# Performance work log

Hardware: AMD Instinct MI355X
Metric: run time of the kernel (lower is better)

Reference implementation:

```python
import jax, jax.numpy as jnp
import numpy as np

B, L, D = 2, 2048, 1024
H, DK, DV = 16, 64, 64
EPS = 1e-6


def setup_inputs() -> dict:
    key = jax.random.key(0)
    ks = jax.random.split(key, 7)
    s = 0.02
    return {
        "x": jax.random.normal(ks[0], (B, L, D), dtype=jnp.float32),
        "Wq": jax.random.normal(ks[1], (D, H * DK), dtype=jnp.float32) * s,
        "Wk": jax.random.normal(ks[2], (D, H * DK), dtype=jnp.float32) * s,
        "Wv": jax.random.normal(ks[3], (D, H * DV), dtype=jnp.float32) * s,
        "Wo": jax.random.normal(ks[4], (H * DV, D), dtype=jnp.float32) * s,
        "ln_gamma": jnp.ones((D,), dtype=jnp.float32),
        "ln_beta": jnp.zeros((D,), dtype=jnp.float32),
    }


def reference(x, Wq, Wk, Wv, Wo, ln_gamma, ln_beta):
    temp = jnp.asarray(DK, x.dtype) ** 0.5
    # projections -> [B, H, L, Dh]
    q = (x @ Wq).reshape(B, L, H, DK).transpose(0, 2, 1, 3)
    k = (x @ Wk).reshape(B, L, H, DK).transpose(0, 2, 1, 3)
    v = (x @ Wv).reshape(B, L, H, DV).transpose(0, 2, 1, 3)
    # naive attention: explicit [B,H,L,L] scores (dropout rate 0 -> identity)
    scores = jnp.einsum("bhqd,bhkd->bhqk", q / temp, k)
    attn = jax.nn.softmax(scores, axis=-1)
    o = jnp.einsum("bhqk,bhkd->bhqd", attn, v)
    o = o.transpose(0, 2, 1, 3).reshape(B, L, H * DV)
    out = o @ Wo + x  # residual
    # LayerNorm(eps=1e-6)
    mu = jnp.mean(out, axis=-1, keepdims=True)
    var = jnp.var(out, axis=-1, keepdims=True)
    return (out - mu) * jax.lax.rsqrt(var + EPS) * ln_gamma + ln_beta
```

## Files before the change

### kernel.cpp

```cpp
#include <hip/hip_runtime.h>


typedef __bf16 bf16;
typedef __bf16 bf16x2 __attribute__((ext_vector_type(2)));
typedef __bf16 bf16x4 __attribute__((ext_vector_type(4)));
typedef __bf16 bf16x8 __attribute__((ext_vector_type(8)));
typedef float floatx4 __attribute__((ext_vector_type(4)));
typedef int intx4 __attribute__((ext_vector_type(4)));

#define MFMA16(a, b, c) __builtin_amdgcn_mfma_f32_16x16x32_bf16((a), (b), (c), 0, 0, 0)

__device__ __forceinline__ void gll16(const bf16* g, bf16* l) {
  __builtin_amdgcn_global_load_lds((const __attribute__((address_space(1))) void*)g,
                                   (__attribute__((address_space(3))) void*)l, 16, 0, 0);
}

__global__ __launch_bounds__(256) void k_prep_x(const float* __restrict__ x, bf16* __restrict__ xb) {
  const int i = (blockIdx.x * 256 + threadIdx.x) * 4;
  const float4 v = *reinterpret_cast<const float4*>(x + i);
  bf16x4 o = {(bf16)v.x, (bf16)v.y, (bf16)v.z, (bf16)v.w};
  *reinterpret_cast<bf16x4*>(xb + i) = o;
}

__global__ __launch_bounds__(256) void k_prep_w(const float* __restrict__ Wq, const float* __restrict__ Wk,
                                                const float* __restrict__ Wv, const float* __restrict__ Wo,
                                                bf16* __restrict__ WT) {
  __shared__ float tile[32][33];
  const int z = blockIdx.z;
  const float* W = (z == 0) ? Wq : (z == 1) ? Wk : (z == 2) ? Wv : Wo;
  const int n0 = blockIdx.x * 32, k0 = blockIdx.y * 32;
  const int tx = threadIdx.x, ty = threadIdx.y;
#pragma unroll
  for (int j = 0; j < 32; j += 8)
    tile[ty + j][tx] = W[(size_t)(k0 + ty + j) * 1024 + n0 + tx];
  __syncthreads();
#pragma unroll
  for (int j = 0; j < 32; j += 8)
    WT[(size_t)(z * 1024 + n0 + ty + j) * 1024 + k0 + tx] = (bf16)tile[tx][ty + j];
}

template <int MODE>
__global__ __launch_bounds__(256) void k_gemm(const bf16* __restrict__ A, const bf16* __restrict__ Bt,
                                              const float* __restrict__ X, float* __restrict__ Y,
                                              bf16* __restrict__ QB, bf16* __restrict__ KB,
                                              bf16* __restrict__ VTB) {
  __shared__ __align__(16) bf16 As[2 * 128 * 64];
  __shared__ __align__(16) bf16 Bs[2 * 128 * 64];
  const int t = threadIdx.x;
  const int lane = t & 63, wv = t >> 6;
  const int qd = lane >> 4, col = lane & 15;
  const int c7 = col & 7;
  const int wm = wv >> 1, wn = wv & 1;
  const int m0 = blockIdx.x * 128, n0 = blockIdx.y * 128;
  const int srow = wv * 8 + (lane >> 3);
  const int scol = ((lane & 7) ^ (lane >> 3)) * 8;
  const bf16* Ag = A + (size_t)(m0 + srow) * 1024 + scol;
  const bf16* Bg = Bt + (size_t)(n0 + srow) * 1024 + scol;

  floatx4 acc[4][4] = {};

#define GSTAGE(ktv, buf)                                                                            \
  do {                                                                                              \
    _Pragma("unroll") for (int rd = 0; rd < 4; rd++) {                                              \
      gll16(Ag + (size_t)rd * 32 * 1024 + (ktv), As + (buf) * 8192 + (rd * 32 + wv * 8) * 64);      \
      gll16(Bg + (size_t)rd * 32 * 1024 + (ktv), Bs + (buf) * 8192 + (rd * 32 + wv * 8) * 64);      \
    }                                                                                               \
  } while (0)

#define GCOMP(buf)                                                                                  \
  do {                                                                                              \
    const bf16* as_ = As + (buf) * 8192;                                                            \
    const bf16* bs_ = Bs + (buf) * 8192;                                                            \
    _Pragma("unroll") for (int ks = 0; ks < 2; ks++) {                                              \
      bf16x8 af[4], bfr[4];                                                                         \
      _Pragma("unroll") for (int i = 0; i < 4; i++)                                                 \
        af[i] = *reinterpret_cast<const bf16x8*>(as_ + (wm * 64 + i * 16 + col) * 64 +              \
                                                 ((ks * 4 + qd) ^ c7) * 8);                         \
      _Pragma("unroll") for (int i = 0; i < 4; i++)                                                 \
        bfr[i] = *reinterpret_cast<const bf16x8*>(bs_ + (wn * 64 + i * 16 + col) * 64 +             \
                                                  ((ks * 4 + qd) ^ c7) * 8);                        \
      _Pragma("unroll") for (int i = 0; i < 4; i++)                                                 \
        _Pragma("unroll") for (int j = 0; j < 4; j++)                                               \
          acc[i][j] = MFMA16(af[i], bfr[j], acc[i][j]);                                             \
    }                                                                                               \
  } while (0)

  GSTAGE(0, 0);
  asm volatile("s_waitcnt vmcnt(0)" ::: "memory");
  __syncthreads();

  for (int kt = 0; kt < 1024; kt += 128) {
    GSTAGE(kt + 64, 1);
    GCOMP(0);
    asm volatile("s_waitcnt vmcnt(0)" ::: "memory");
    __syncthreads();
    if (kt + 128 < 1024) GSTAGE(kt + 128, 0);
    GCOMP(1);
    asm volatile("s_waitcnt vmcnt(0)" ::: "memory");
    __syncthreads();
  }
#undef GSTAGE
#undef GCOMP

#pragma unroll
  for (int i = 0; i < 4; i++) {
#pragma unroll
    for (int j = 0; j < 4; j++) {
      const int mb = m0 + wm * 64 + i * 16 + qd * 4;
      const int n = n0 + wn * 64 + j * 16 + col;
      if (MODE == 0) {
        const int seg = n >> 10;
        const int h = (n & 1023) >> 6, dd = n & 63;
#pragma unroll
        for (int r = 0; r < 4; r++) {
          const int m = mb + r;
          const int bb = m >> 11, l = m & 2047;
          const float v = acc[i][j][r];
          if (seg == 0)
            QB[((size_t)(bb * 16 + h) * 2048 + l) * 64 + dd] = (bf16)(v * 0.18033688f);
          else if (seg == 1)
            KB[((size_t)(bb * 16 + h) * 2048 + l) * 64 + dd] = (bf16)v;
          else
            VTB[((size_t)(bb * 16 + h) * 64 + dd) * 2048 + l] = (bf16)v;
        }
      } else {
#pragma unroll
        for (int r = 0; r < 4; r++) {
          const int m = mb + r;
          Y[(size_t)m * 1024 + n] = acc[i][j][r] + X[(size_t)m * 1024 + n];
        }
      }
    }
  }
}

__global__ __launch_bounds__(256) void k_attn(const bf16* __restrict__ QB, const bf16* __restrict__ KB,
                                              const bf16* __restrict__ VTB, bf16* __restrict__ PO0,
                                              bf16* __restrict__ PO1, float* __restrict__ LS) {
  __shared__ __align__(16) bf16 Ks[3][64 * 64];
  __shared__ __align__(16) bf16 Vs[3][64 * 64];
  const int t = threadIdx.x;
  const int lane = t & 63, wv = t >> 6;
  const int qd = lane >> 4, col = lane & 15;
  const int c7 = col & 7;
  const int bh = blockIdx.y;
  const int z = blockIdx.z;
  const int qr = blockIdx.x * 128 + wv * 32;
  const int lrow0 = wv * 8 + (lane >> 3);
  const int scol = ((lane & 7) ^ (lane >> 3)) * 8;
  const int kg0 = ((lrow0 >> 5) << 5) + (((lrow0 >> 2) & 3) << 3) + (((lrow0 >> 4) & 1) << 2) + (lrow0 & 3);
  const int r1 = lrow0 + 32;
  const int kg1 = ((r1 >> 5) << 5) + (((r1 >> 2) & 3) << 3) + (((r1 >> 4) & 1) << 2) + (r1 & 3);
  const bf16* Kg0 = KB + ((size_t)bh * 2048 + kg0) * 64 + scol;
  const bf16* Kg1 = KB + ((size_t)bh * 2048 + kg1) * 64 + scol;
  const bf16* Vg0 = VTB + ((size_t)bh * 64 + lrow0) * 2048 + scol;
  const bf16* Vg1 = VTB + ((size_t)bh * 64 + lrow0 + 32) * 2048 + scol;

  bf16x8 bQ[2][2];
#pragma unroll
  for (int qt = 0; qt < 2; qt++)
#pragma unroll
    for (int s = 0; s < 2; s++)
      bQ[qt][s] = *reinterpret_cast<const bf16x8*>(QB + ((size_t)bh * 2048 + qr + qt * 16 + col) * 64 + s * 32 + qd * 8);

  floatx4 oacc[2][4] = {};
  float lsum[2] = {0.f, 0.f};
  floatx4 scur[2][4];
  int pk[2][4][2];

#define STAGE(bu, ti)                                                  \
  do {                                                                 \
    gll16(Kg0 + (size_t)(ti) * 4096, &Ks[bu][(wv * 8) * 64]);          \
    gll16(Kg1 + (size_t)(ti) * 4096, &Ks[bu][(32 + wv * 8) * 64]);     \
    gll16(Vg0 + (ti) * 64, &Vs[bu][(wv * 8) * 64]);                    \
    gll16(Vg1 + (ti) * 64, &Vs[bu][(32 + wv * 8) * 64]);               \
  } while (0)

#define QK(bu)                                                                                      \
  do {                                                                                              \
    const bf16* ks_ = Ks[bu];                                                                       \
    _Pragma("unroll") for (int nt = 0; nt < 4; nt++) {                                              \
      bf16x8 a0 = *reinterpret_cast<const bf16x8*>(ks_ + (nt * 16 + col) * 64 + (qd ^ c7) * 8);     \
      bf16x8 a1 = *reinterpret_cast<const bf16x8*>(ks_ + (nt * 16 + col) * 64 + ((4 + qd) ^ c7) * 8); \
      _Pragma("unroll") for (int qt = 0; qt < 2; qt++) {                                            \
        floatx4 zz = {0.f, 0.f, 0.f, 0.f};                                                          \
        zz = MFMA16(a0, bQ[qt][0], zz);                                                             \
        zz = MFMA16(a1, bQ[qt][1], zz);                                                             \
        scur[qt][nt] = zz;                                                                          \
      }                                                                                             \
    }                                                                                               \
  } while (0)

#define EXPPACK()                                                                               \
  do {                                                                                          \
    _Pragma("unroll") for (int qt = 0; qt < 2; qt++) {                                          \
      _Pragma("unroll") for (int nt = 0; nt < 4; nt++) {                                        \
        const float e0 = __builtin_amdgcn_exp2f(scur[qt][nt][0]);                               \
        const float e1 = __builtin_amdgcn_exp2f(scur[qt][nt][1]);                               \
        const float e2 = __builtin_amdgcn_exp2f(scur[qt][nt][2]);                               \
        const float e3 = __builtin_amdgcn_exp2f(scur[qt][nt][3]);                               \
        lsum[qt] += (e0 + e1) + (e2 + e3);                                                      \
        bf16x2 p01, p23;                                                                        \
        p01[0] = (bf16)e0; p01[1] = (bf16)e1;                                                   \
        p23[0] = (bf16)e2; p23[1] = (bf16)e3;                                                   \
        pk[qt][nt][0] = __builtin_bit_cast(int, p01);                                           \
        pk[qt][nt][1] = __builtin_bit_cast(int, p23);                                           \
      }                                                                                         \
    }                                                                                           \
  } while (0)

#define PV(bu)                                                                                      \
  do {                                                                                              \
    const bf16* vs_ = Vs[bu];                                                                       \
    bf16x8 bV[4][2];                                                                                \
    _Pragma("unroll") for (int nd = 0; nd < 4; nd++) {                                              \
      bV[nd][0] = *reinterpret_cast<const bf16x8*>(vs_ + (nd * 16 + col) * 64 + (qd ^ c7) * 8);     \
      bV[nd][1] = *reinterpret_cast<const bf16x8*>(vs_ + (nd * 16 + col) * 64 + ((4 + qd) ^ c7) * 8); \
    }                                                                                               \
    _Pragma("unroll") for (int qt = 0; qt < 2; qt++) {                                              \
      _Pragma("unroll") for (int s = 0; s < 2; s++) {                                               \
        intx4 w;                                                                                    \
        w[0] = pk[qt][2 * s][0]; w[1] = pk[qt][2 * s][1];                                           \
        w[2] = pk[qt][2 * s + 1][0]; w[3] = pk[qt][2 * s + 1][1];                                   \
        const bf16x8 aP = __builtin_bit_cast(bf16x8, w);                                            \
        _Pragma("unroll") for (int nd = 0; nd < 4; nd++)                                            \
          oacc[qt][nd] = MFMA16(aP, bV[nd][s], oacc[qt][nd]);                                       \
      }                                                                                             \
    }                                                                                               \
  } while (0)

#define ITER(cur, prv, ti)                                             \
  do {                                                                 \
    asm volatile("s_waitcnt vmcnt(4)" ::: "memory");                   \
    __builtin_amdgcn_s_barrier();                                      \
    EXPPACK();                                                         \
    QK(cur);                                                           \
    PV(prv);                                                           \
    __builtin_amdgcn_s_barrier();                                      \
    STAGE(prv, ((ti) + 2 <= t0 + 15) ? ((ti) + 2) : (t0 + 15));        \
  } while (0)

  const int t0 = z * 16;
  STAGE(0, t0);
  STAGE(1, t0 + 1);
  asm volatile("s_waitcnt vmcnt(4)" ::: "memory");
  __builtin_amdgcn_s_barrier();
  QK(0);
  __builtin_amdgcn_s_barrier();
  STAGE(2, t0 + 2);
  for (int j = 1; j < 16; j += 3) {
    ITER(1, 0, t0 + j);
    ITER(2, 1, t0 + j + 1);
    ITER(0, 2, t0 + j + 2);
  }
  EXPPACK();
  PV(0);

#pragma unroll
  for (int qt = 0; qt < 2; qt++) {
    lsum[qt] += __shfl_xor(lsum[qt], 16);
    lsum[qt] += __shfl_xor(lsum[qt], 32);
  }
  if (qd == 0) {
#pragma unroll
    for (int qt = 0; qt < 2; qt++)
      LS[(size_t)z * 65536 + (size_t)bh * 2048 + qr + qt * 16 + col] = lsum[qt];
  }
  bf16* PO = z ? PO1 : PO0;
  const int bb = bh >> 4, h = bh & 15;
#pragma unroll
  for (int qt = 0; qt < 2; qt++) {
#pragma unroll
    for (int r = 0; r < 4; r++) {
      const size_t m = (size_t)bb * 2048 + qr + qt * 16 + qd * 4 + r;
#pragma unroll
      for (int nd = 0; nd < 4; nd++)
        PO[m * 1024 + h * 64 + nd * 16 + col] = (bf16)(oacc[qt][nd][r]);
    }
  }
#undef STAGE
#undef QK
#undef EXPPACK
#undef PV
#undef ITER
}

__global__ __launch_bounds__(256) void k_comb(const bf16* __restrict__ PO0, const bf16* __restrict__ PO1,
                                              const float* __restrict__ LS, bf16* __restrict__ OB) {
  const size_t idx = ((size_t)blockIdx.x * 256 + threadIdx.x) * 4;
  const int m = (int)(idx >> 10), c = (int)(idx & 1023);
  const int bb = m >> 11, l = m & 2047, h = c >> 6;
  const int bh = bb * 16 + h;
  const float linv = 1.f / (LS[(size_t)bh * 2048 + l] + LS[65536 + (size_t)bh * 2048 + l]);
  const bf16x4 a = *reinterpret_cast<const bf16x4*>(PO0 + idx);
  const bf16x4 b = *reinterpret_cast<const bf16x4*>(PO1 + idx);
  bf16x4 o;
#pragma unroll
  for (int i = 0; i < 4; i++) o[i] = (bf16)(((float)a[i] + (float)b[i]) * linv);
  *reinterpret_cast<bf16x4*>(OB + idx) = o;
}

__global__ __launch_bounds__(256) void k_ln(const float* __restrict__ Yin, const float* __restrict__ gamma,
                                            const float* __restrict__ beta, float* __restrict__ out) {
  __shared__ float red[8];
  const int row = blockIdx.x, t = threadIdx.x;
  const float4 v = *reinterpret_cast<const float4*>(Yin + (size_t)row * 1024 + t * 4);
  float s = v.x + v.y + v.z + v.w;
  float ss = v.x * v.x + v.y * v.y + v.z * v.z + v.w * v.w;
#pragma unroll
  for (int d = 1; d < 64; d <<= 1) {
    s += __shfl_xor(s, d);
    ss += __shfl_xor(ss, d);
  }
  if ((t & 63) == 0) {
    red[t >> 6] = s;
    red[4 + (t >> 6)] = ss;
  }
  __syncthreads();
  s = red[0] + red[1] + red[2] + red[3];
  ss = red[4] + red[5] + red[6] + red[7];
  const float mu = s * (1.f / 1024.f);
  const float var = ss * (1.f / 1024.f) - mu * mu;
  const float rs = rsqrtf(var + 1e-6f);
  const float4 g = *reinterpret_cast<const float4*>(gamma + t * 4);
  const float4 bt = *reinterpret_cast<const float4*>(beta + t * 4);
  float4 o;
  o.x = (v.x - mu) * rs * g.x + bt.x;
  o.y = (v.y - mu) * rs * g.y + bt.y;
  o.z = (v.z - mu) * rs * g.z + bt.z;
  o.w = (v.w - mu) * rs * g.w + bt.w;
  *reinterpret_cast<float4*>(out + (size_t)row * 1024 + t * 4) = o;
}

extern "C" void kernel_launch(void* const* d_in, const int* in_sizes, int n_in,
                              void* d_out, int out_size, void* d_ws, size_t ws_size,
                              hipStream_t stream) {
  (void)in_sizes; (void)n_in; (void)out_size; (void)ws_size;
  const float* x = (const float*)d_in[0];
  const float* Wq = (const float*)d_in[1];
  const float* Wk = (const float*)d_in[2];
  const float* Wv = (const float*)d_in[3];
  const float* Wo = (const float*)d_in[4];
  const float* gamma = (const float*)d_in[5];
  const float* beta = (const float*)d_in[6];

  char* ws = (char*)d_ws;
  const size_t MB = 1ull << 20;
  bf16* XB = (bf16*)(ws);
  bf16* PO0 = (bf16*)(ws);
  bf16* OB = (bf16*)(ws);
  bf16* WT = (bf16*)(ws + 8 * MB);
  bf16* QB = (bf16*)(ws + 16 * MB);
  bf16* KB = (bf16*)(ws + 24 * MB);
  bf16* VTB = (bf16*)(ws + 32 * MB);
  bf16* PO1 = (bf16*)(ws + 40 * MB);
  float* LS = (float*)(ws + 48 * MB);
  float* Y = (float*)(ws + 16 * MB);

  k_prep_x<<<4096, 256, 0, stream>>>(x, XB);
  k_prep_w<<<dim3(32, 32, 4), dim3(32, 8), 0, stream>>>(Wq, Wk, Wv, Wo, WT);
  k_gemm<0><<<dim3(32, 24), 256, 0, stream>>>(XB, WT, nullptr, nullptr, QB, KB, VTB);
  k_attn<<<dim3(16, 32, 2), 256, 0, stream>>>(QB, KB, VTB, PO0, PO1, LS);
  k_comb<<<4096, 256, 0, stream>>>(PO0, PO1, LS, OB);
  k_gemm<1><<<dim3(32, 8), 256, 0, stream>>>(OB, WT + (size_t)3072 * 1024, x, Y,
                                             nullptr, nullptr, nullptr);
  k_ln<<<4096, 256, 0, stream>>>(Y, gamma, beta, (float*)d_out);
}
```

Before: 215.3 us.

## Triple-buffer GEMM K-loop and drop split-K attention combine pass

The GEMM main loop moves from a double-buffered scheme with full vmcnt(0) waits to a three-stage ring buffer that keeps one tile load in flight during compute, with partial waits and raw barriers. The attention kernel no longer splits the key range across two blocks. Each block now walks all 32 key tiles and normalises the output directly, which removes the partial-output writes, the LS buffer and the separate combine kernel. In exchange the attention grid is half as large, giving less parallelism per launch, and the GEMM uses more LDS, which may reduce occupancy.

```diff
diff --git a/kernel.cpp b/kernel.cpp
--- a/kernel.cpp
+++ b/kernel.cpp
@@ -44,8 +44,8 @@
                                               const float* __restrict__ X, float* __restrict__ Y,
                                               bf16* __restrict__ QB, bf16* __restrict__ KB,
                                               bf16* __restrict__ VTB) {
-  __shared__ __align__(16) bf16 As[2 * 128 * 64];
-  __shared__ __align__(16) bf16 Bs[2 * 128 * 64];
+  __shared__ __align__(16) bf16 As[3 * 128 * 64];
+  __shared__ __align__(16) bf16 Bs[3 * 128 * 64];
   const int t = threadIdx.x;
   const int lane = t & 63, wv = t >> 6;
   const int qd = lane >> 4, col = lane & 15;
@@ -59,18 +59,18 @@
 
   floatx4 acc[4][4] = {};
 
-#define GSTAGE(ktv, buf)                                                                            \
+#define GSTAGE(bu, ti)                                                                              \
   do {                                                                                              \
     _Pragma("unroll") for (int rd = 0; rd < 4; rd++) {                                              \
-      gll16(Ag + (size_t)rd * 32 * 1024 + (ktv), As + (buf) * 8192 + (rd * 32 + wv * 8) * 64);      \
-      gll16(Bg + (size_t)rd * 32 * 1024 + (ktv), Bs + (buf) * 8192 + (rd * 32 + wv * 8) * 64);      \
-    }                                                                                               \
-  } while (0)
-
-#define GCOMP(buf)                                                                                  \
+      gll16(Ag + (size_t)rd * 32 * 1024 + (ti) * 64, As + (bu) * 8192 + (rd * 32 + wv * 8) * 64);   \
+      gll16(Bg + (size_t)rd * 32 * 1024 + (ti) * 64, Bs + (bu) * 8192 + (rd * 32 + wv * 8) * 64);   \
+    }                                                                                               \
+  } while (0)
+
+#define GCOMP(bu)                                                                                   \
   do {                                                                                              \
-    const bf16* as_ = As + (buf) * 8192;                                                            \
-    const bf16* bs_ = Bs + (buf) * 8192;                                                            \
+    const bf16* as_ = As + (bu) * 8192;                                                             \
+    const bf16* bs_ = Bs + (bu) * 8192;                                                             \
     _Pragma("unroll") for (int ks = 0; ks < 2; ks++) {                                              \
       bf16x8 af[4], bfr[4];                                                                         \
       _Pragma("unroll") for (int i = 0; i < 4; i++)                                                 \
@@ -85,22 +85,30 @@
     }                                                                                               \
   } while (0)
 
+#define GITER(cur, prv, ti)                                            \
+  do {                                                                 \
+    asm volatile("s_waitcnt vmcnt(8)" ::: "memory");                   \
+    __builtin_amdgcn_s_barrier();                                      \
+    GCOMP(cur);                                                        \
+    __builtin_amdgcn_s_barrier();                                      \
+    GSTAGE(prv, ((ti) + 2 <= 15) ? ((ti) + 2) : 15);                   \
+  } while (0)
+
   GSTAGE(0, 0);
-  asm volatile("s_waitcnt vmcnt(0)" ::: "memory");
-  __syncthreads();
-
-  for (int kt = 0; kt < 1024; kt += 128) {
-    GSTAGE(kt + 64, 1);
-    GCOMP(0);
-    asm volatile("s_waitcnt vmcnt(0)" ::: "memory");
-    __syncthreads();
-    if (kt + 128 < 1024) GSTAGE(kt + 128, 0);
-    GCOMP(1);
-    asm volatile("s_waitcnt vmcnt(0)" ::: "memory");
-    __syncthreads();
+  GSTAGE(1, 1);
+  asm volatile("s_waitcnt vmcnt(8)" ::: "memory");
+  __builtin_amdgcn_s_barrier();
+  GCOMP(0);
+  __builtin_amdgcn_s_barrier();
+  GSTAGE(2, 2);
+  for (int j = 1; j < 16; j += 3) {
+    GITER(1, 0, j);
+    GITER(2, 1, j + 1);
+    GITER(0, 2, j + 2);
   }
 #undef GSTAGE
 #undef GCOMP
+#undef GITER
 
 #pragma unroll
   for (int i = 0; i < 4; i++) {
@@ -135,8 +143,7 @@
 }
 
 __global__ __launch_bounds__(256) void k_attn(const bf16* __restrict__ QB, const bf16* __restrict__ KB,
-                                              const bf16* __restrict__ VTB, bf16* __restrict__ PO0,
-                                              bf16* __restrict__ PO1, float* __restrict__ LS) {
+                                              const bf16* __restrict__ VTB, bf16* __restrict__ OB) {
   __shared__ __align__(16) bf16 Ks[3][64 * 64];
   __shared__ __align__(16) bf16 Vs[3][64 * 64];
   const int t = threadIdx.x;
@@ -144,7 +151,6 @@
   const int qd = lane >> 4, col = lane & 15;
   const int c7 = col & 7;
   const int bh = blockIdx.y;
-  const int z = blockIdx.z;
   const int qr = blockIdx.x * 128 + wv * 32;
   const int lrow0 = wv * 8 + (lane >> 3);
   const int scol = ((lane & 7) ^ (lane >> 3)) * 8;
@@ -237,45 +243,40 @@
     QK(cur);                                                           \
     PV(prv);                                                           \
     __builtin_amdgcn_s_barrier();                                      \
-    STAGE(prv, ((ti) + 2 <= t0 + 15) ? ((ti) + 2) : (t0 + 15));        \
-  } while (0)
-
-  const int t0 = z * 16;
-  STAGE(0, t0);
-  STAGE(1, t0 + 1);
+    STAGE(prv, ((ti) + 2 <= 31) ? ((ti) + 2) : 31);                    \
+  } while (0)
+
+  STAGE(0, 0);
+  STAGE(1, 1);
   asm volatile("s_waitcnt vmcnt(4)" ::: "memory");
   __builtin_amdgcn_s_barrier();
   QK(0);
   __builtin_amdgcn_s_barrier();
-  STAGE(2, t0 + 2);
-  for (int j = 1; j < 16; j += 3) {
-    ITER(1, 0, t0 + j);
-    ITER(2, 1, t0 + j + 1);
-    ITER(0, 2, t0 + j + 2);
-  }
+  STAGE(2, 2);
+  for (int j = 1; j < 30; j += 3) {
+    ITER(1, 0, j);
+    ITER(2, 1, j + 1);
+    ITER(0, 2, j + 2);
+  }
+  ITER(1, 0, 31);
   EXPPACK();
-  PV(0);
+  PV(1);
 
 #pragma unroll
   for (int qt = 0; qt < 2; qt++) {
     lsum[qt] += __shfl_xor(lsum[qt], 16);
     lsum[qt] += __shfl_xor(lsum[qt], 32);
   }
-  if (qd == 0) {
-#pragma unroll
-    for (int qt = 0; qt < 2; qt++)
-      LS[(size_t)z * 65536 + (size_t)bh * 2048 + qr + qt * 16 + col] = lsum[qt];
-  }
-  bf16* PO = z ? PO1 : PO0;
   const int bb = bh >> 4, h = bh & 15;
 #pragma unroll
   for (int qt = 0; qt < 2; qt++) {
 #pragma unroll
     for (int r = 0; r < 4; r++) {
+      const float linv = 1.f / __shfl(lsum[qt], qd * 4 + r);
       const size_t m = (size_t)bb * 2048 + qr + qt * 16 + qd * 4 + r;
 #pragma unroll
       for (int nd = 0; nd < 4; nd++)
-        PO[m * 1024 + h * 64 + nd * 16 + col] = (bf16)(oacc[qt][nd][r]);
+        OB[m * 1024 + h * 64 + nd * 16 + col] = (bf16)(oacc[qt][nd][r] * linv);
     }
   }
 #undef STAGE
@@ -283,21 +284,6 @@
 #undef EXPPACK
 #undef PV
 #undef ITER
-}
-
-__global__ __launch_bounds__(256) void k_comb(const bf16* __restrict__ PO0, const bf16* __restrict__ PO1,
-                                              const float* __restrict__ LS, bf16* __restrict__ OB) {
-  const size_t idx = ((size_t)blockIdx.x * 256 + threadIdx.x) * 4;
-  const int m = (int)(idx >> 10), c = (int)(idx & 1023);
-  const int bb = m >> 11, l = m & 2047, h = c >> 6;
-  const int bh = bb * 16 + h;
-  const float linv = 1.f / (LS[(size_t)bh * 2048 + l] + LS[65536 + (size_t)bh * 2048 + l]);
-  const bf16x4 a = *reinterpret_cast<const bf16x4*>(PO0 + idx);
-  const bf16x4 b = *reinterpret_cast<const bf16x4*>(PO1 + idx);
-  bf16x4 o;
-#pragma unroll
-  for (int i = 0; i < 4; i++) o[i] = (bf16)(((float)a[i] + (float)b[i]) * linv);
-  *reinterpret_cast<bf16x4*>(OB + idx) = o;
 }
 
 __global__ __launch_bounds__(256) void k_ln(const float* __restrict__ Yin, const float* __restrict__ gamma,
@@ -347,21 +333,17 @@
   char* ws = (char*)d_ws;
   const size_t MB = 1ull << 20;
   bf16* XB = (bf16*)(ws);
-  bf16* PO0 = (bf16*)(ws);
   bf16* OB = (bf16*)(ws);
   bf16* WT = (bf16*)(ws + 8 * MB);
   bf16* QB = (bf16*)(ws + 16 * MB);
   bf16* KB = (bf16*)(ws + 24 * MB);
   bf16* VTB = (bf16*)(ws + 32 * MB);
-  bf16* PO1 = (bf16*)(ws + 40 * MB);
-  float* LS = (float*)(ws + 48 * MB);
   float* Y = (float*)(ws + 16 * MB);
 
   k_prep_x<<<4096, 256, 0, stream>>>(x, XB);
   k_prep_w<<<dim3(32, 32, 4), dim3(32, 8), 0, stream>>>(Wq, Wk, Wv, Wo, WT);
   k_gemm<0><<<dim3(32, 24), 256, 0, stream>>>(XB, WT, nullptr, nullptr, QB, KB, VTB);
-  k_attn<<<dim3(16, 32, 2), 256, 0, stream>>>(QB, KB, VTB, PO0, PO1, LS);
-  k_comb<<<4096, 256, 0, stream>>>(PO0, PO1, LS, OB);
+  k_attn<<<dim3(16, 32), 256, 0, stream>>>(QB, KB, VTB, OB);
   k_gemm<1><<<dim3(32, 8), 256, 0, stream>>>(OB, WT + (size_t)3072 * 1024, x, Y,
                                              nullptr, nullptr, nullptr);
   k_ln<<<4096, 256, 0, stream>>>(Y, gamma, beta, (float*)d_out);
```

New measurement: 210.1 us. -2.5%, faster.
